# Kernel optimization log

Hardware: AMD Instinct MI355X
Metric: run time of the kernel (lower is better)

## Reference

```python
import jax, jax.numpy as jnp
import numpy as np

T, B, D_IN, R, D_OUT = 256, 64, 512, 2048, 128
SPARSITY, BETA, THRESH = 0.8, 0.9, 1.0


def setup_inputs() -> dict:
    key = jax.random.key(0)
    ks = jax.random.split(key, 6)
    lim_rec = float(np.sqrt(3.0 / R))  # VarianceScaling(1.0,'fan_avg','uniform') with fan_in=fan_out=R
    return {
        "x_seq": jax.random.normal(ks[0], (T, B, D_IN), jnp.float32),
        "w_in": jax.random.normal(ks[1], (D_IN, R), jnp.float32) / np.sqrt(D_IN).astype(np.float32),
        "b_in": jnp.zeros((R,), jnp.float32),
        "w_rec": jax.random.uniform(ks[2], (R, R), jnp.float32, -lim_rec, lim_rec),
        "w_head": jax.random.normal(ks[3], (R, D_OUT), jnp.float32) / np.sqrt(R).astype(np.float32),
        "b_head": jnp.zeros((D_OUT,), jnp.float32),
    }


def reference(x_seq, w_in, b_in, w_rec, w_head, b_head):
    n = R * R
    keep = max(1, int(n * (1.0 - SPARSITY)))
    scores = jnp.abs(w_rec).reshape(-1)
    thresh = jnp.sort(scores)[n - keep]  # k-th largest of |w_rec| (same threshold as top_k)
    mask = (jnp.abs(w_rec) >= thresh).astype(w_rec.dtype)
    w_eff = w_rec * mask

    # input projection is time-parallel; hoist it out of the scan
    drive_in = jnp.einsum('tbd,dr->tbr', x_seq, w_in) + b_in  # [T,B,R]

    def step(carry, drive_t):
        V, prev_s = carry
        cur = drive_t + prev_s @ w_eff          # sparse recurrent drive
        V = BETA * V + cur                      # LIF integrate (leak + input)
        s = (V > THRESH).astype(x_seq.dtype)    # heaviside spike
        V = V - s * THRESH                      # soft reset
        logits = s @ w_head + b_head
        return (V, s), (logits, jnp.mean(s))

    init = (jnp.zeros((B, R), x_seq.dtype), jnp.zeros((B, R), x_seq.dtype))
    _, (logits_seq, sr_seq) = jax.lax.scan(step, init, drive_in)

    readout = jnp.mean(logits_seq, axis=0)  # readout mode 'mean'
    spike_rate = jnp.asarray([jnp.mean(sr_seq)])
    active_ratio = jnp.mean(mask)
    return readout, logits_seq, spike_rate, active_ratio
```

## Files before the change

kernel.cpp:

```cpp
#include <hip/hip_runtime.h>
#include <hip/hip_bf16.h>
#include <stdint.h>

#define TT 256
#define BB 64
#define DIN 512
#define RR 2048
#define DOUT 128
#define NTOT (RR*RR)
#define NKEEP 838860
#define BETA 0.9f
#define VTH 1.0f


__global__ void k_init(uint32_t* __restrict__ p, int n) {
    int i = blockIdx.x * blockDim.x + threadIdx.x;
    int stride = gridDim.x * blockDim.x;
    for (; i < n; i += stride) p[i] = 0u;
}

__global__ void k_hist(const float* __restrict__ w_rec, uint32_t* __restrict__ hist,
                       const uint32_t* __restrict__ state, int p) {
    __shared__ uint32_t lh[256];
    lh[threadIdx.x] = 0u;
    __syncthreads();
    uint32_t prefix = (p > 0) ? state[0] : 0u;
    int sh = 24 - 8 * p;
    int i = blockIdx.x * 256 + threadIdx.x;
    int stride = gridDim.x * 256;
    for (; i < NTOT; i += stride) {
        uint32_t u = __float_as_uint(fabsf(w_rec[i]));
        bool ok = (p == 0) || ((u >> (sh + 8)) == prefix);
        if (ok) atomicAdd(&lh[(u >> sh) & 255u], 1u);
    }
    __syncthreads();
    uint32_t v = lh[threadIdx.x];
    if (v) atomicAdd(&hist[threadIdx.x], v);
}

__global__ void k_select(uint32_t* __restrict__ hist, uint32_t* __restrict__ state, int p) {
    __shared__ uint32_t lh[256];
    int tid = threadIdx.x;
    lh[tid] = hist[tid];
    hist[tid] = 0u;
    __syncthreads();
    if (tid == 0) {
        uint32_t remaining = (p == 0) ? (uint32_t)NKEEP : state[1];
        int bin = 255;
        for (; bin > 0; --bin) {
            uint32_t c = lh[bin];
            if (c >= remaining) break;
            remaining -= c;
        }
        uint32_t pref = (p == 0) ? 0u : state[0];
        pref = (pref << 8) | (uint32_t)bin;
        state[0] = pref;
        state[1] = remaining;
        if (p == 3) state[2] = pref;
    }
}

__global__ void k_maskcount(float* __restrict__ w, const uint32_t* __restrict__ state,
                            uint32_t* __restrict__ cnts) {
    uint32_t th = state[2];
    uint32_t c = 0;
    int i = blockIdx.x * blockDim.x + threadIdx.x;
    int stride = gridDim.x * blockDim.x;
    for (; i < NTOT / 4; i += stride) {
        float4 v = *(float4*)&w[i * 4];
        if ((__float_as_uint(v.x) & 0x7fffffffu) >= th) c++; else v.x = 0.0f;
        if ((__float_as_uint(v.y) & 0x7fffffffu) >= th) c++; else v.y = 0.0f;
        if ((__float_as_uint(v.z) & 0x7fffffffu) >= th) c++; else v.z = 0.0f;
        if ((__float_as_uint(v.w) & 0x7fffffffu) >= th) c++; else v.w = 0.0f;
        *(float4*)&w[i * 4] = v;
    }
    for (int off = 32; off > 0; off >>= 1) c += __shfl_down(c, off);
    if ((threadIdx.x & 63) == 0 && c) atomicAdd(&cnts[1], c);
}

__global__ __launch_bounds__(256) void k_drive(const float* __restrict__ x,
                                               const float* __restrict__ w_in,
                                               const float* __restrict__ b_in,
                                               float* __restrict__ drive) {
    __shared__ float As[8][128];
    __shared__ float Bs[8][128];
    const int m0 = blockIdx.x * 128;
    const int n0 = blockIdx.y * 128;
    const int tid = threadIdx.x;
    const int tx = tid & 15, ty = tid >> 4;
    const int ar = tid >> 1;
    const int ak = (tid & 1) * 4;
    const int bk = tid >> 5;
    const int bc = (tid & 31) * 4;
    float acc[8][8];
    #pragma unroll
    for (int i = 0; i < 8; ++i)
        #pragma unroll
        for (int j = 0; j < 8; ++j) acc[i][j] = 0.0f;

    for (int k0 = 0; k0 < DIN; k0 += 8) {
        float4 av = *(const float4*)&x[(m0 + ar) * DIN + k0 + ak];
        float4 bv = *(const float4*)&w_in[(size_t)(k0 + bk) * RR + n0 + bc];
        __syncthreads();
        As[ak + 0][ar] = av.x; As[ak + 1][ar] = av.y;
        As[ak + 2][ar] = av.z; As[ak + 3][ar] = av.w;
        *(float4*)&Bs[bk][bc] = bv;
        __syncthreads();
        #pragma unroll
        for (int kk = 0; kk < 8; ++kk) {
            float a[8], b[8];
            *(float4*)&a[0] = *(const float4*)&As[kk][ty * 8];
            *(float4*)&a[4] = *(const float4*)&As[kk][ty * 8 + 4];
            *(float4*)&b[0] = *(const float4*)&Bs[kk][tx * 8];
            *(float4*)&b[4] = *(const float4*)&Bs[kk][tx * 8 + 4];
            #pragma unroll
            for (int i = 0; i < 8; ++i)
                #pragma unroll
                for (int j = 0; j < 8; ++j)
                    acc[i][j] = fmaf(a[i], b[j], acc[i][j]);
        }
    }
    float bb[8];
    #pragma unroll
    for (int j = 0; j < 8; ++j) bb[j] = b_in[n0 + tx * 8 + j];
    #pragma unroll
    for (int i = 0; i < 8; ++i) {
        size_t row = (size_t)(m0 + ty * 8 + i) * RR + n0 + tx * 8;
        float4 v0, v1;
        v0.x = acc[i][0] + bb[0]; v0.y = acc[i][1] + bb[1];
        v0.z = acc[i][2] + bb[2]; v0.w = acc[i][3] + bb[3];
        v1.x = acc[i][4] + bb[4]; v1.y = acc[i][5] + bb[5];
        v1.z = acc[i][6] + bb[6]; v1.w = acc[i][7] + bb[7];
        *(float4*)&drive[row] = v0;
        *(float4*)&drive[row + 4] = v1;
    }
}

__global__ __launch_bounds__(256) void k_scan(const float* __restrict__ w_rec,
                                              const float* __restrict__ drive,
                                              uint32_t* mask, unsigned long long* flags,
                                              uint32_t* cnts) {
    __shared__ __align__(16) int s_list[RR];
    __shared__ int s_n;
    __shared__ uint32_t s_red[4];

    const int tid = threadIdx.x;
    const int blk = blockIdx.x;
    const int cg = blk & 7;
    const int b = blk >> 3;
    const int col = (cg << 8) + tid;
    const int w = tid >> 6;
    const int lane = tid & 63;
    const char* Wp = (const char*)(w_rec + col);

    float V = 0.f;
    uint32_t scnt = 0;
    float dv = drive[(size_t)b * RR + col];

    for (int t = 0; t < TT; ++t) {
        float a = dv;
        if (t > 0) {
            if (tid == 0) {
                const unsigned long long* fl = &flags[(size_t)(t - 1) * BB + b];
                while (__hip_atomic_load(fl, __ATOMIC_RELAXED, __HIP_MEMORY_SCOPE_AGENT)
                       != ~0ull)
                    __builtin_amdgcn_s_sleep(1);
            }
            __syncthreads();
            if (tid < 64) {
                uint32_t m = __hip_atomic_load(&mask[((size_t)(t - 1) * BB + b) * 64 + tid],
                                               __ATOMIC_RELAXED, __HIP_MEMORY_SCOPE_AGENT);
                int p = __popc(m);
                int off = p;
                #pragma unroll
                for (int d = 1; d < 64; d <<= 1) {
                    int o = __shfl_up(off, d);
                    if (tid >= d) off += o;
                }
                if (tid == 63) s_n = off;
                int e = off - p;
                int base = tid << 5;
                while (m) {
                    int bit = __builtin_ctz(m);
                    m &= m - 1;
                    s_list[e++] = (base + bit) << 13;
                }
            }
            __syncthreads();
            const int n = s_n;
            int i = 0;
            for (; i + 16 <= n; i += 16) {
                int4 o0 = *(const int4*)&s_list[i];
                int4 o1 = *(const int4*)&s_list[i + 4];
                int4 o2 = *(const int4*)&s_list[i + 8];
                int4 o3 = *(const int4*)&s_list[i + 12];
                float v[16];
                v[0]  = *(const float*)(Wp + o0.x);
                v[1]  = *(const float*)(Wp + o0.y);
                v[2]  = *(const float*)(Wp + o0.z);
                v[3]  = *(const float*)(Wp + o0.w);
                v[4]  = *(const float*)(Wp + o1.x);
                v[5]  = *(const float*)(Wp + o1.y);
                v[6]  = *(const float*)(Wp + o1.z);
                v[7]  = *(const float*)(Wp + o1.w);
                v[8]  = *(const float*)(Wp + o2.x);
                v[9]  = *(const float*)(Wp + o2.y);
                v[10] = *(const float*)(Wp + o2.z);
                v[11] = *(const float*)(Wp + o2.w);
                v[12] = *(const float*)(Wp + o3.x);
                v[13] = *(const float*)(Wp + o3.y);
                v[14] = *(const float*)(Wp + o3.z);
                v[15] = *(const float*)(Wp + o3.w);
                #pragma unroll
                for (int j = 0; j < 16; ++j) a += v[j];
            }
            for (; i + 4 <= n; i += 4) {
                int4 o = *(const int4*)&s_list[i];
                float v0 = *(const float*)(Wp + o.x);
                float v1 = *(const float*)(Wp + o.y);
                float v2 = *(const float*)(Wp + o.z);
                float v3 = *(const float*)(Wp + o.w);
                a += v0; a += v1; a += v2; a += v3;
            }
            for (; i < n; ++i) a += *(const float*)(Wp + s_list[i]);
        }

        V = BETA * V + a;
        bool sp = V > VTH;
        if (sp) V -= VTH;

        if (t + 1 < TT)
            dv = drive[((size_t)(t + 1) * BB + b) * RR + col];

        unsigned long long bal = __ballot(sp);
        if (lane == 0) {
            __hip_atomic_store(
                (unsigned long long*)&mask[((size_t)t * BB + b) * 64] + (cg * 4 + w),
                bal, __ATOMIC_RELAXED, __HIP_MEMORY_SCOPE_AGENT);
            scnt += (uint32_t)__popcll(bal);
        }
        __syncthreads();
        if (tid == 0)
            __hip_atomic_store((uint8_t*)&flags[(size_t)t * BB + b] + cg, (uint8_t)0xFF,
                               __ATOMIC_RELEASE, __HIP_MEMORY_SCOPE_AGENT);
    }

    if (lane == 0) s_red[w] = scnt;
    __syncthreads();
    if (tid == 0) {
        uint32_t s = s_red[0] + s_red[1] + s_red[2] + s_red[3];
        if (s) atomicAdd(&cnts[0], s);
    }
}

__global__ __launch_bounds__(128) void k_head(const uint32_t* __restrict__ mask,
                                              const float* __restrict__ w_head,
                                              const float* __restrict__ b_head,
                                              float* __restrict__ logits) {
    __shared__ __align__(16) int s_list[RR];
    __shared__ int s_n;
    int tb = blockIdx.x;
    int tid = threadIdx.x;
    if (tid < 64) {
        uint32_t m = mask[tb * 64 + tid];
        int p = __popc(m);
        int off = p;
        #pragma unroll
        for (int d = 1; d < 64; d <<= 1) {
            int o = __shfl_up(off, d);
            if (tid >= d) off += o;
        }
        if (tid == 63) s_n = off;
        int e = off - p;
        int base = tid << 5;
        while (m) {
            int bit = __builtin_ctz(m);
            m &= m - 1;
            s_list[e++] = (base + bit) << 9;
        }
    }
    __syncthreads();
    const char* Wp = (const char*)(w_head + tid);
    float acc = b_head[tid];
    const int n = s_n;
    int i = 0;
    for (; i + 8 <= n; i += 8) {
        int4 o0 = *(const int4*)&s_list[i];
        int4 o1 = *(const int4*)&s_list[i + 4];
        float v[8];
        v[0] = *(const float*)(Wp + o0.x);
        v[1] = *(const float*)(Wp + o0.y);
        v[2] = *(const float*)(Wp + o0.z);
        v[3] = *(const float*)(Wp + o0.w);
        v[4] = *(const float*)(Wp + o1.x);
        v[5] = *(const float*)(Wp + o1.y);
        v[6] = *(const float*)(Wp + o1.z);
        v[7] = *(const float*)(Wp + o1.w);
        #pragma unroll
        for (int j = 0; j < 8; ++j) acc += v[j];
    }
    for (; i < n; ++i) acc += *(const float*)(Wp + s_list[i]);
    logits[(size_t)tb * DOUT + tid] = acc;
}

__global__ __launch_bounds__(128) void k_readout(const float* __restrict__ logits,
                                                 float* __restrict__ readout) {
    int b = blockIdx.x, cidx = threadIdx.x;
    float s = 0.0f;
    for (int t = 0; t < TT; ++t)
        s += logits[(size_t)t * (BB * DOUT) + b * DOUT + cidx];
    readout[b * DOUT + cidx] = s * (1.0f / (float)TT);
}

__global__ void k_scalars(const uint32_t* __restrict__ cnts, float* __restrict__ out) {
    if (threadIdx.x == 0 && blockIdx.x == 0) {
        out[BB * DOUT + TT * BB * DOUT]     = (float)cnts[0] / (float)(TT * BB * RR);
        out[BB * DOUT + TT * BB * DOUT + 1] = (float)cnts[1] / (float)NTOT;
    }
}

extern "C" void kernel_launch(void* const* d_in, const int* in_sizes, int n_in,
                              void* d_out, int out_size, void* d_ws, size_t ws_size,
                              hipStream_t stream) {
    const float* x      = (const float*)d_in[0];
    const float* w_in   = (const float*)d_in[1];
    const float* b_in   = (const float*)d_in[2];
    float*       w_rec  = (float*)d_in[3];
    const float* w_head = (const float*)d_in[4];
    const float* b_head = (const float*)d_in[5];
    float* out = (float*)d_out;

    float*    drive = (float*)d_ws;
    uint32_t* mask  = (uint32_t*)((char*)d_ws + 134217728u);
    unsigned long long* flags = (unsigned long long*)(mask + (TT * BB * 64));
    uint32_t* hist  = (uint32_t*)(flags + TT * BB);
    uint32_t* state = hist + 256;
    uint32_t* cnts  = state + 8;

    k_init<<<64, 256, 0, stream>>>((uint32_t*)flags, TT * BB * 2 + 256 + 8 + 2);

    for (int p = 0; p < 4; ++p) {
        k_hist<<<1024, 256, 0, stream>>>(w_rec, hist, state, p);
        k_select<<<1, 256, 0, stream>>>(hist, state, p);
    }
    k_maskcount<<<1024, 256, 0, stream>>>(w_rec, state, cnts);

    k_drive<<<dim3(128, 16), 256, 0, stream>>>(x, w_in, b_in, drive);

    k_scan<<<512, 256, 0, stream>>>(w_rec, drive, mask, flags, cnts);

    k_head<<<TT * BB, 128, 0, stream>>>(mask, w_head, b_head, out + BB * DOUT);
    k_readout<<<BB, 128, 0, stream>>>(out + BB * DOUT, out);
    k_scalars<<<1, 64, 0, stream>>>(cnts, out);
}
```

Before: 4.881 ms.

## Pad scan flags per cache line, deepen gather unroll, defer drive prefetch

Pads each per-timestep/batch flag word to its own 128-byte slot so spinning blocks do not share cache lines with flags other blocks are writing. Adds a 64-wide gather batch with a scheduling barrier in the recurrent scan, and widens the head gather to 16 loads, so more memory loads are in flight. Moves the next-step drive load after the flag release so the release is not held back by it, and adds a launch bound of 2 blocks per SM. Costs more register pressure and a larger flag-init area.

```diff
diff --git a/kernel.cpp b/kernel.cpp
--- a/kernel.cpp
+++ b/kernel.cpp
@@ -12,6 +12,8 @@
 #define BETA 0.9f
 #define VTH 1.0f
 
+
+#define FLAG_STRIDE 16
 
 __global__ void k_init(uint32_t* __restrict__ p, int n) {
     int i = blockIdx.x * blockDim.x + threadIdx.x;
@@ -136,10 +138,10 @@
     }
 }
 
-__global__ __launch_bounds__(256) void k_scan(const float* __restrict__ w_rec,
-                                              const float* __restrict__ drive,
-                                              uint32_t* mask, unsigned long long* flags,
-                                              uint32_t* cnts) {
+__global__ __launch_bounds__(256, 2) void k_scan(const float* __restrict__ w_rec,
+                                                 const float* __restrict__ drive,
+                                                 uint32_t* mask, unsigned long long* flags,
+                                                 uint32_t* cnts) {
     __shared__ __align__(16) int s_list[RR];
     __shared__ int s_n;
     __shared__ uint32_t s_red[4];
@@ -161,7 +163,8 @@
         float a = dv;
         if (t > 0) {
             if (tid == 0) {
-                const unsigned long long* fl = &flags[(size_t)(t - 1) * BB + b];
+                const unsigned long long* fl =
+                    &flags[(size_t)((t - 1) * BB + b) * FLAG_STRIDE];
                 while (__hip_atomic_load(fl, __ATOMIC_RELAXED, __HIP_MEMORY_SCOPE_AGENT)
                        != ~0ull)
                     __builtin_amdgcn_s_sleep(1);
@@ -189,28 +192,31 @@
             __syncthreads();
             const int n = s_n;
             int i = 0;
+            for (; i + 64 <= n; i += 64) {
+                float v[64];
+                #pragma unroll
+                for (int u = 0; u < 64; u += 4) {
+                    int4 o = *(const int4*)&s_list[i + u];
+                    v[u + 0] = *(const float*)(Wp + o.x);
+                    v[u + 1] = *(const float*)(Wp + o.y);
+                    v[u + 2] = *(const float*)(Wp + o.z);
+                    v[u + 3] = *(const float*)(Wp + o.w);
+                }
+                __builtin_amdgcn_sched_barrier(0);
+                #pragma unroll
+                for (int j = 0; j < 64; ++j) a += v[j];
+            }
             for (; i + 16 <= n; i += 16) {
-                int4 o0 = *(const int4*)&s_list[i];
-                int4 o1 = *(const int4*)&s_list[i + 4];
-                int4 o2 = *(const int4*)&s_list[i + 8];
-                int4 o3 = *(const int4*)&s_list[i + 12];
                 float v[16];
-                v[0]  = *(const float*)(Wp + o0.x);
-                v[1]  = *(const float*)(Wp + o0.y);
-                v[2]  = *(const float*)(Wp + o0.z);
-                v[3]  = *(const float*)(Wp + o0.w);
-                v[4]  = *(const float*)(Wp + o1.x);
-                v[5]  = *(const float*)(Wp + o1.y);
-                v[6]  = *(const float*)(Wp + o1.z);
-                v[7]  = *(const float*)(Wp + o1.w);
-                v[8]  = *(const float*)(Wp + o2.x);
-                v[9]  = *(const float*)(Wp + o2.y);
-                v[10] = *(const float*)(Wp + o2.z);
-                v[11] = *(const float*)(Wp + o2.w);
-                v[12] = *(const float*)(Wp + o3.x);
-                v[13] = *(const float*)(Wp + o3.y);
-                v[14] = *(const float*)(Wp + o3.z);
-                v[15] = *(const float*)(Wp + o3.w);
+                #pragma unroll
+                for (int u = 0; u < 16; u += 4) {
+                    int4 o = *(const int4*)&s_list[i + u];
+                    v[u + 0] = *(const float*)(Wp + o.x);
+                    v[u + 1] = *(const float*)(Wp + o.y);
+                    v[u + 2] = *(const float*)(Wp + o.z);
+                    v[u + 3] = *(const float*)(Wp + o.w);
+                }
+                __builtin_amdgcn_sched_barrier(0);
                 #pragma unroll
                 for (int j = 0; j < 16; ++j) a += v[j];
             }
@@ -229,9 +235,6 @@
         bool sp = V > VTH;
         if (sp) V -= VTH;
 
-        if (t + 1 < TT)
-            dv = drive[((size_t)(t + 1) * BB + b) * RR + col];
-
         unsigned long long bal = __ballot(sp);
         if (lane == 0) {
             __hip_atomic_store(
@@ -241,8 +244,12 @@
         }
         __syncthreads();
         if (tid == 0)
-            __hip_atomic_store((uint8_t*)&flags[(size_t)t * BB + b] + cg, (uint8_t)0xFF,
-                               __ATOMIC_RELEASE, __HIP_MEMORY_SCOPE_AGENT);
+            __hip_atomic_store(
+                (uint8_t*)&flags[(size_t)(t * BB + b) * FLAG_STRIDE] + cg, (uint8_t)0xFF,
+                __ATOMIC_RELEASE, __HIP_MEMORY_SCOPE_AGENT);
+        __builtin_amdgcn_sched_barrier(0);
+        if (t + 1 < TT)
+            dv = drive[((size_t)(t + 1) * BB + b) * RR + col];
     }
 
     if (lane == 0) s_red[w] = scnt;
@@ -284,20 +291,19 @@
     float acc = b_head[tid];
     const int n = s_n;
     int i = 0;
-    for (; i + 8 <= n; i += 8) {
-        int4 o0 = *(const int4*)&s_list[i];
-        int4 o1 = *(const int4*)&s_list[i + 4];
-        float v[8];
-        v[0] = *(const float*)(Wp + o0.x);
-        v[1] = *(const float*)(Wp + o0.y);
-        v[2] = *(const float*)(Wp + o0.z);
-        v[3] = *(const float*)(Wp + o0.w);
-        v[4] = *(const float*)(Wp + o1.x);
-        v[5] = *(const float*)(Wp + o1.y);
-        v[6] = *(const float*)(Wp + o1.z);
-        v[7] = *(const float*)(Wp + o1.w);
-        #pragma unroll
-        for (int j = 0; j < 8; ++j) acc += v[j];
+    for (; i + 16 <= n; i += 16) {
+        float v[16];
+        #pragma unroll
+        for (int u = 0; u < 16; u += 4) {
+            int4 o = *(const int4*)&s_list[i + u];
+            v[u + 0] = *(const float*)(Wp + o.x);
+            v[u + 1] = *(const float*)(Wp + o.y);
+            v[u + 2] = *(const float*)(Wp + o.z);
+            v[u + 3] = *(const float*)(Wp + o.w);
+        }
+        __builtin_amdgcn_sched_barrier(0);
+        #pragma unroll
+        for (int j = 0; j < 16; ++j) acc += v[j];
     }
     for (; i < n; ++i) acc += *(const float*)(Wp + s_list[i]);
     logits[(size_t)tb * DOUT + tid] = acc;
@@ -333,11 +339,12 @@
     float*    drive = (float*)d_ws;
     uint32_t* mask  = (uint32_t*)((char*)d_ws + 134217728u);
     unsigned long long* flags = (unsigned long long*)(mask + (TT * BB * 64));
-    uint32_t* hist  = (uint32_t*)(flags + TT * BB);
+    uint32_t* hist  = (uint32_t*)(flags + (size_t)TT * BB * FLAG_STRIDE);
     uint32_t* state = hist + 256;
     uint32_t* cnts  = state + 8;
 
-    k_init<<<64, 256, 0, stream>>>((uint32_t*)flags, TT * BB * 2 + 256 + 8 + 2);
+    k_init<<<256, 256, 0, stream>>>((uint32_t*)flags,
+                                    TT * BB * FLAG_STRIDE * 2 + 256 + 8 + 2);
 
     for (int p = 0; p < 4; ++p) {
         k_hist<<<1024, 256, 0, stream>>>(w_rec, hist, state, p);
```

Result: faster. 4.280 ms (median of 2 runs) (-12.3%).
